# Optimization experiments

Hardware: AMD Instinct MI355X
Metric: run time of the kernel (lower is better)

## Reference

```python
import jax, jax.numpy as jnp
import numpy as np

NEG_BIG = -9e15
ALPHA = 0.2  # LeakyReLU negative slope


def setup_inputs() -> dict:
    key = jax.random.key(0)
    k_h, k_adj, k_W, k_a = jax.random.split(key, 4)
    B, N, F_in, F_out = 16, 2048, 128, 64
    h = jax.random.normal(k_h, (B, N, F_in), dtype=jnp.float32)
    adj = jax.random.randint(k_adj, (B, N, N), 0, 2).astype(jnp.float32)
    mask = jnp.ones((B, N, 1), dtype=jnp.float32)
    W = jax.random.normal(k_W, (F_in, F_out), dtype=jnp.float32) * (1.0 / np.sqrt(F_in))
    a = jax.random.normal(k_a, (2 * F_out, 1), dtype=jnp.float32) * (1.0 / np.sqrt(2 * F_out))
    return {"h": h, "adj": adj, "mask": mask, "W": W, "a": a}


def reference(h, adj, mask, W, a):
    # h: [B,N,Fi], adj: [B,N,N], mask: [B,N,1], W: [Fi,Fo], a: [2Fo,1]
    F_out = W.shape[1]
    Wh = jnp.einsum("bnf,fo->bno", h, W)  # [B,N,Fo]
    # concat(Wh_i, Wh_j) @ a == (Wh @ a_src)_i + (Wh @ a_dst)_j  -- avoids O(B N^2 2Fo) tensor
    a_src = a[:F_out, 0]
    a_dst = a[F_out:, 0]
    f_i = Wh @ a_src  # [B,N]
    f_j = Wh @ a_dst  # [B,N]
    e = jax.nn.leaky_relu(f_i[:, :, None] + f_j[:, None, :], negative_slope=ALPHA)  # [B,N,N]
    node_mask = mask[..., 0]  # [B,N]
    edge_mask = (adj > 0).astype(e.dtype) * node_mask[:, None, :] * node_mask[:, :, None]
    attn_logits = jnp.where(edge_mask > 0, e, jnp.full_like(e, NEG_BIG))
    attention = jax.nn.softmax(attn_logits, axis=2)  # dropout p=0 -> identity
    h_prime = jnp.einsum("bij,bjo->bio", attention, Wh)  # [B,N,Fo]
    return jax.nn.relu(h_prime)
```

## Files before the change

kernel.cpp:

```cpp
#include <hip/hip_runtime.h>
#include <stdint.h>


#define BB   16
#define NN   2048
#define FIN  128
#define FO   64
#define LOG2E 1.4426950408889634f

typedef float v4f __attribute__((ext_vector_type(4)));
typedef short v8s __attribute__((ext_vector_type(8)));
typedef int   v4i __attribute__((ext_vector_type(4)));
typedef unsigned int u32;

__device__ __forceinline__ int pack_bf16(float e0, float e1) {
    unsigned u0 = __float_as_uint(e0) + 0x8000u;
    unsigned u1 = __float_as_uint(e1) + 0x8000u;
    return (int)__builtin_amdgcn_perm(u1, u0, 0x07060302u);
}

__device__ __forceinline__ void gload16(const void* g, void* l) {
    __builtin_amdgcn_global_load_lds(
        (const __attribute__((address_space(1))) u32*)g,
        (__attribute__((address_space(3))) u32*)l, 16, 0, 0);
}

__global__ __launch_bounds__(128) void k_wh(
    const float* __restrict__ h, const float* __restrict__ W,
    const float* __restrict__ a,
    float* __restrict__ fsl2, float* __restrict__ fdl2,
    unsigned short* __restrict__ whT)
{
    __shared__ float Wlds[FIN * FO];
    __shared__ float hs[64 * 129];

    const int t  = threadIdx.x;
    const int b  = blockIdx.y;
    const int n0 = blockIdx.x * 64;

    {
        const v4f* Wg = (const v4f*)W;
        v4f* Wl = (v4f*)Wlds;
        #pragma unroll
        for (int i = 0; i < 16; ++i) Wl[t + 128 * i] = Wg[t + 128 * i];
    }
    {
        const v4f* hg = (const v4f*)(h + ((size_t)b * NN + n0) * FIN);
        #pragma unroll
        for (int i = 0; i < 16; ++i) {
            int idx = t + 128 * i;
            v4f v = __builtin_nontemporal_load(hg + idx);
            int r = idx >> 5;
            int c = (idx & 31) * 4;
            float* d = &hs[r * 129 + c];
            d[0] = v[0]; d[1] = v[1]; d[2] = v[2]; d[3] = v[3];
        }
    }
    __syncthreads();

    const int rg = t & 15;
    const int og = t >> 4;

    float acc[4][8];
    #pragma unroll
    for (int r = 0; r < 4; ++r)
        #pragma unroll
        for (int k = 0; k < 8; ++k) acc[r][k] = 0.f;

    #pragma unroll 2
    for (int f = 0; f < FIN; ++f) {
        float hv[4];
        #pragma unroll
        for (int r = 0; r < 4; ++r) hv[r] = hs[(rg * 4 + r) * 129 + f];
        const v4f* wr = (const v4f*)&Wlds[f * FO + og * 8];
        v4f w0 = wr[0];
        v4f w1 = wr[1];
        #pragma unroll
        for (int r = 0; r < 4; ++r) {
            acc[r][0] += hv[r] * w0[0]; acc[r][1] += hv[r] * w0[1];
            acc[r][2] += hv[r] * w0[2]; acc[r][3] += hv[r] * w0[3];
            acc[r][4] += hv[r] * w1[0]; acc[r][5] += hv[r] * w1[1];
            acc[r][6] += hv[r] * w1[2]; acc[r][7] += hv[r] * w1[3];
        }
    }

    float fs[4] = {0.f, 0.f, 0.f, 0.f};
    float fd[4] = {0.f, 0.f, 0.f, 0.f};
    #pragma unroll
    for (int k = 0; k < 8; ++k) {
        float as = a[og * 8 + k];
        float ad = a[FO + og * 8 + k];
        #pragma unroll
        for (int r = 0; r < 4; ++r) {
            fs[r] += acc[r][k] * as;
            fd[r] += acc[r][k] * ad;
        }
    }
    __syncthreads();
    #pragma unroll
    for (int r = 0; r < 4; ++r) {
        hs[og * 64 + rg * 4 + r]       = fs[r];
        hs[512 + og * 64 + rg * 4 + r] = fd[r];
    }
    __syncthreads();
    if (t < 64) {
        float s = 0.f, d2 = 0.f;
        #pragma unroll
        for (int g = 0; g < 8; ++g) {
            s  += hs[g * 64 + t];
            d2 += hs[512 + g * 64 + t];
        }
        fsl2[b * NN + n0 + t] = s  * LOG2E;
        fdl2[b * NN + n0 + t] = d2 * LOG2E;
    }

    #pragma unroll
    for (int k = 0; k < 8; ++k) {
        int o = og * 8 + k;
        int2 pk;
        pk.x = pack_bf16(acc[0][k], acc[1][k]);
        pk.y = pack_bf16(acc[2][k], acc[3][k]);
        *(int2*)&whT[((size_t)b * FO + o) * NN + n0 + rg * 4] = pk;
    }
}

__global__ __launch_bounds__(256, 3) void k_attn(
    const float* __restrict__ adj, const float* __restrict__ fsl2,
    const float* __restrict__ fdl2,
    const unsigned short* __restrict__ whT, float* __restrict__ out)
{
    __shared__ char smem[8192 + 2 * 16384];

    const int t    = threadIdx.x;
    const int lane = t & 63;
    const int wv   = t >> 6;
    const int lin  = blockIdx.x;
    const int xcd  = lin & 7;
    const int s    = lin >> 3;
    const int b    = xcd * 2 + (s >> 7);
    const int itile = s & 127;
    const int i_base = itile * 16;
    const int m    = lane & 15;
    const int quad = lane >> 4;
    const int l    = lane;

    const float fil2 = fsl2[b * NN + i_base + m];
    {
        const v4f* fg = (const v4f*)(fdl2 + b * NN);
        v4f* fl = (v4f*)smem;
        fl[t]       = fg[t];
        fl[t + 256] = fg[t + 256];
    }

    const int r0 = wv * 4;
    const float* aS0 = adj + ((size_t)(b * NN + i_base + r0    )) * NN + ((l ^ (r0    )) << 2);
    const float* aS1 = adj + ((size_t)(b * NN + i_base + r0 + 1)) * NN + ((l ^ (r0 + 1)) << 2);
    const float* aS2 = adj + ((size_t)(b * NN + i_base + r0 + 2)) * NN + ((l ^ (r0 + 2)) << 2);
    const float* aS3 = adj + ((size_t)(b * NN + i_base + r0 + 3)) * NN + ((l ^ (r0 + 3)) << 2);

    char* slot0 = smem + 8192;
    char* slot1 = smem + 8192 + 16384;
    const int d0 = (r0    ) * 1024 + l * 16;
    const int d1 = (r0 + 1) * 1024 + l * 16;
    const int d2 = (r0 + 2) * 1024 + l * 16;
    const int d3 = (r0 + 3) * 1024 + l * 16;

    const unsigned short* wfp = whT + (size_t)b * FO * NN
                              + (size_t)(wv * 16 + m) * NN + quad * 8;

    const int mbase = m * 1024;
    const int qm2   = quad * 2;

    gload16(aS0, slot0 + d0);
    gload16(aS1, slot0 + d1);
    gload16(aS2, slot0 + d2);
    gload16(aS3, slot0 + d3);
    __syncthreads();

    v4i onesi = {0x3F803F80, 0x3F803F80, 0x3F803F80, 0x3F803F80};
    v8s onesf = __builtin_bit_cast(v8s, onesi);

    v4f acc  = {0.f, 0.f, 0.f, 0.f};
    v4f accs = {0.f, 0.f, 0.f, 0.f};

    for (int c = 0; c < 8; ++c) {
        asm volatile("s_waitcnt vmcnt(0)" ::: "memory");
        __builtin_amdgcn_s_barrier();
        __builtin_amdgcn_sched_barrier(0);

        v8s fr[8];
        #pragma unroll
        for (int js = 0; js < 8; ++js)
            fr[js] = *(const v8s*)(wfp + c * 256 + js * 32);
        __builtin_amdgcn_sched_barrier(0);

        if (c < 7) {
            char* sl = (c & 1) ? slot0 : slot1;
            gload16(aS0 + (c + 1) * 256, sl + d0);
            gload16(aS1 + (c + 1) * 256, sl + d1);
            gload16(aS2 + (c + 1) * 256, sl + d2);
            gload16(aS3 + (c + 1) * 256, sl + d3);
        }
        __builtin_amdgcn_sched_barrier(0);

        const char* ab = (c & 1) ? slot1 : slot0;

        #pragma unroll
        for (int js = 0; js < 8; ++js) {
            const int u = js * 8 + qm2;
            v4f A0 = *(const v4f*)(ab + mbase + (((u    ) ^ m) << 4));
            v4f A1 = *(const v4f*)(ab + mbase + (((u + 1) ^ m) << 4));
            v4f F0 = *(const v4f*)(smem + c * 1024 + js * 128 + quad * 32);
            v4f F1 = *(const v4f*)(smem + c * 1024 + js * 128 + quad * 32 + 16);

            float w[8];
            #pragma unroll
            for (int e = 0; e < 8; ++e) {
                float av = (e < 4) ? A0[e] : A1[e - 4];
                float fv = (e < 4) ? F0[e] : F1[e - 4];
                float sc = fil2 + fv;
                float lr = fmaxf(sc, 0.2f * sc);
                w[e] = av * __builtin_amdgcn_exp2f(lr);
            }
            v4i pk;
            pk.x = pack_bf16(w[0], w[1]);
            pk.y = pack_bf16(w[2], w[3]);
            pk.z = pack_bf16(w[4], w[5]);
            pk.w = pack_bf16(w[6], w[7]);
            v8s afrag = __builtin_bit_cast(v8s, pk);

            acc  = __builtin_amdgcn_mfma_f32_16x16x32_bf16(afrag, fr[js], acc,  0, 0, 0);
            accs = __builtin_amdgcn_mfma_f32_16x16x32_bf16(afrag, onesf,  accs, 0, 0, 0);
        }
    }

    #pragma unroll
    for (int r = 0; r < 4; ++r) {
        float dl = accs[r];
        float inv = dl > 0.f ? 1.0f / dl : 0.f;
        size_t ro = ((size_t)(b * NN + i_base + quad * 4 + r)) * FO + wv * 16 + m;
        __builtin_nontemporal_store(fmaxf(acc[r] * inv, 0.f), out + ro);
    }
}

extern "C" void kernel_launch(void* const* d_in, const int* in_sizes, int n_in,
                              void* d_out, int out_size, void* d_ws, size_t ws_size,
                              hipStream_t stream)
{
    const float* h   = (const float*)d_in[0];
    const float* adj = (const float*)d_in[1];
    const float* W   = (const float*)d_in[3];
    const float* a   = (const float*)d_in[4];
    float* out = (float*)d_out;

    char* ws = (char*)d_ws;
    float* fsl2 = (float*)ws;
    float* fdl2 = (float*)(ws + 131072);
    unsigned short* whT = (unsigned short*)(ws + 262144);

    k_wh  <<<dim3(NN / 64, BB), 128, 0, stream>>>(h, W, a, fsl2, fdl2, whT);
    k_attn<<<dim3(2048),        256, 0, stream>>>(adj, fsl2, fdl2, whT, out);
}
```

Before: 406.8 us.

## Deepen adjacency LDS pipeline to four slots and prefetch value fragments

The attention kernel's adjacency staging grows from a double buffer to a four-slot ring with three chunks in flight. The whT bf16 fragments are now loaded one chunk ahead into alternating register sets. The loop is fully unrolled with explicit vmcnt thresholds instead of draining to zero each iteration. The aim is more memory-level parallelism on the latency-bound adjacency stream, at the cost of more LDS per block and a min-blocks launch bound lowered from 3 to 2. The hand-picked vmcnt counts must exactly match the in-order issue of loads; if they are off, adjacency data could be read before it has arrived.

```diff
diff --git a/kernel.cpp b/kernel.cpp
--- a/kernel.cpp
+++ b/kernel.cpp
@@ -124,12 +124,12 @@
     }
 }
 
-__global__ __launch_bounds__(256, 3) void k_attn(
+__global__ __launch_bounds__(256, 2) void k_attn(
     const float* __restrict__ adj, const float* __restrict__ fsl2,
     const float* __restrict__ fdl2,
     const unsigned short* __restrict__ whT, float* __restrict__ out)
 {
-    __shared__ char smem[8192 + 2 * 16384];
+    __shared__ char smem[8192 + 4 * 16384];
 
     const int t    = threadIdx.x;
     const int lane = t & 63;
@@ -158,8 +158,7 @@
     const float* aS2 = adj + ((size_t)(b * NN + i_base + r0 + 2)) * NN + ((l ^ (r0 + 2)) << 2);
     const float* aS3 = adj + ((size_t)(b * NN + i_base + r0 + 3)) * NN + ((l ^ (r0 + 3)) << 2);
 
-    char* slot0 = smem + 8192;
-    char* slot1 = smem + 8192 + 16384;
+    char* Asl = smem + 8192;
     const int d0 = (r0    ) * 1024 + l * 16;
     const int d1 = (r0 + 1) * 1024 + l * 16;
     const int d2 = (r0 + 2) * 1024 + l * 16;
@@ -171,11 +170,19 @@
     const int mbase = m * 1024;
     const int qm2   = quad * 2;
 
-    gload16(aS0, slot0 + d0);
-    gload16(aS1, slot0 + d1);
-    gload16(aS2, slot0 + d2);
-    gload16(aS3, slot0 + d3);
-    __syncthreads();
+#define STAGE(cn) do {                                            \
+        char* sl_ = Asl + ((cn) & 3) * 16384;                     \
+        gload16(aS0 + (cn) * 256, sl_ + d0);                      \
+        gload16(aS1 + (cn) * 256, sl_ + d1);                      \
+        gload16(aS2 + (cn) * 256, sl_ + d2);                      \
+        gload16(aS3 + (cn) * 256, sl_ + d3);                      \
+    } while (0)
+
+#define FRAGS(cn, FR) do {                                        \
+        _Pragma("unroll")                                         \
+        for (int js = 0; js < 8; ++js)                            \
+            FR[js] = *(const v8s*)(wfp + (cn) * 256 + js * 32);   \
+    } while (0)
 
     v4i onesi = {0x3F803F80, 0x3F803F80, 0x3F803F80, 0x3F803F80};
     v8s onesf = __builtin_bit_cast(v8s, onesi);
@@ -183,56 +190,69 @@
     v4f acc  = {0.f, 0.f, 0.f, 0.f};
     v4f accs = {0.f, 0.f, 0.f, 0.f};
 
-    for (int c = 0; c < 8; ++c) {
-        asm volatile("s_waitcnt vmcnt(0)" ::: "memory");
-        __builtin_amdgcn_s_barrier();
-        __builtin_amdgcn_sched_barrier(0);
-
-        v8s fr[8];
-        #pragma unroll
-        for (int js = 0; js < 8; ++js)
-            fr[js] = *(const v8s*)(wfp + c * 256 + js * 32);
-        __builtin_amdgcn_sched_barrier(0);
-
-        if (c < 7) {
-            char* sl = (c & 1) ? slot0 : slot1;
-            gload16(aS0 + (c + 1) * 256, sl + d0);
-            gload16(aS1 + (c + 1) * 256, sl + d1);
-            gload16(aS2 + (c + 1) * 256, sl + d2);
-            gload16(aS3 + (c + 1) * 256, sl + d3);
-        }
-        __builtin_amdgcn_sched_barrier(0);
-
-        const char* ab = (c & 1) ? slot1 : slot0;
-
-        #pragma unroll
-        for (int js = 0; js < 8; ++js) {
-            const int u = js * 8 + qm2;
-            v4f A0 = *(const v4f*)(ab + mbase + (((u    ) ^ m) << 4));
-            v4f A1 = *(const v4f*)(ab + mbase + (((u + 1) ^ m) << 4));
-            v4f F0 = *(const v4f*)(smem + c * 1024 + js * 128 + quad * 32);
-            v4f F1 = *(const v4f*)(smem + c * 1024 + js * 128 + quad * 32 + 16);
-
-            float w[8];
-            #pragma unroll
-            for (int e = 0; e < 8; ++e) {
-                float av = (e < 4) ? A0[e] : A1[e - 4];
-                float fv = (e < 4) ? F0[e] : F1[e - 4];
-                float sc = fil2 + fv;
-                float lr = fmaxf(sc, 0.2f * sc);
-                w[e] = av * __builtin_amdgcn_exp2f(lr);
-            }
-            v4i pk;
-            pk.x = pack_bf16(w[0], w[1]);
-            pk.y = pack_bf16(w[2], w[3]);
-            pk.z = pack_bf16(w[4], w[5]);
-            pk.w = pack_bf16(w[6], w[7]);
-            v8s afrag = __builtin_bit_cast(v8s, pk);
-
-            acc  = __builtin_amdgcn_mfma_f32_16x16x32_bf16(afrag, fr[js], acc,  0, 0, 0);
-            accs = __builtin_amdgcn_mfma_f32_16x16x32_bf16(afrag, onesf,  accs, 0, 0, 0);
-        }
-    }
+#define COMP(c_, FR) do {                                                      \
+        const char* ab_ = Asl + ((c_) & 3) * 16384;                            \
+        _Pragma("unroll")                                                      \
+        for (int js = 0; js < 8; ++js) {                                       \
+            const int u = js * 8 + qm2;                                        \
+            v4f A0 = *(const v4f*)(ab_ + mbase + (((u    ) ^ m) << 4));        \
+            v4f A1 = *(const v4f*)(ab_ + mbase + (((u + 1) ^ m) << 4));        \
+            v4f F0 = *(const v4f*)(smem + (c_) * 1024 + js * 128 + quad * 32); \
+            v4f F1 = *(const v4f*)(smem + (c_) * 1024 + js * 128 + quad * 32 + 16); \
+            float w[8];                                                        \
+            _Pragma("unroll")                                                  \
+            for (int e = 0; e < 8; ++e) {                                      \
+                float av = (e < 4) ? A0[e] : A1[e - 4];                        \
+                float fv = (e < 4) ? F0[e] : F1[e - 4];                        \
+                float sc = fil2 + fv;                                          \
+                float lr = fmaxf(sc, 0.2f * sc);                               \
+                w[e] = av * __builtin_amdgcn_exp2f(lr);                        \
+            }                                                                  \
+            v4i pk;                                                            \
+            pk.x = pack_bf16(w[0], w[1]);                                      \
+            pk.y = pack_bf16(w[2], w[3]);                                      \
+            pk.z = pack_bf16(w[4], w[5]);                                      \
+            pk.w = pack_bf16(w[6], w[7]);                                      \
+            v8s afrag = __builtin_bit_cast(v8s, pk);                           \
+            acc  = __builtin_amdgcn_mfma_f32_16x16x32_bf16(afrag, FR[js], acc,  0, 0, 0); \
+            accs = __builtin_amdgcn_mfma_f32_16x16x32_bf16(afrag, onesf,  accs, 0, 0, 0); \
+        }                                                                      \
+    } while (0)
+
+    v8s frA[8], frB[8];
+
+    STAGE(0);
+    STAGE(1);
+    STAGE(2);
+    FRAGS(0, frA);
+    __syncthreads();
+
+#define ITER(c_, K_, FRcur, FRnext, DOFRAG, DOADJ) do {           \
+        asm volatile("s_waitcnt vmcnt(" #K_ ")" ::: "memory");    \
+        __builtin_amdgcn_sched_barrier(0);                        \
+        __builtin_amdgcn_s_barrier();                             \
+        __builtin_amdgcn_sched_barrier(0);                        \
+        if (DOFRAG) { FRAGS((c_) + 1, FRnext); }                  \
+        __builtin_amdgcn_sched_barrier(0);                        \
+        if (DOADJ) { STAGE((c_) + 3); }                           \
+        __builtin_amdgcn_sched_barrier(0);                        \
+        COMP(c_, FRcur);                                          \
+        __builtin_amdgcn_sched_barrier(0);                        \
+    } while (0)
+
+    ITER(0, 24, frA, frB, 1, 1);
+    ITER(1, 24, frB, frA, 1, 1);
+    ITER(2, 24, frA, frB, 1, 1);
+    ITER(3, 24, frB, frA, 1, 1);
+    ITER(4, 24, frA, frB, 1, 1);
+    ITER(5, 24, frB, frA, 1, 0);
+    ITER(6, 20, frA, frB, 1, 0);
+    ITER(7, 16, frB, frA, 0, 0);
+
+#undef ITER
+#undef COMP
+#undef FRAGS
+#undef STAGE
 
     #pragma unroll
     for (int r = 0; r < 4; ++r) {
```

Result: no change. 413.4 us (+1.6%).
